# Optimization experiments

Hardware: AMD Instinct MI355X
Metric: run time of the kernel (lower is better)

Reference implementation:

```python
import jax, jax.numpy as jnp
import numpy as np

N = 1_000_000      # level-0 points
M = 50_000         # level-1 superpoints
G = 16             # graphs in batch (norm_index groups)
DIMS = (32, 128, 64)
EPS = 1e-5
NEG_SLOPE = 0.01   # torch nn.LeakyReLU default


def graph_norm(x, idx, gamma, beta, num_graphs):
    """Per-graph batch norm ('graph' mode): normalize each feature channel
    using mean/var computed over the nodes of each graph (segment)."""
    cnt = jax.ops.segment_sum(jnp.ones((x.shape[0],), x.dtype), idx, num_segments=num_graphs)
    cnt = jnp.maximum(cnt, 1.0)[:, None]                       # [G,1]
    mean = jax.ops.segment_sum(x, idx, num_segments=num_graphs) / cnt      # [G,D]
    ex2 = jax.ops.segment_sum(x * x, idx, num_segments=num_graphs) / cnt   # [G,D]
    var = jnp.maximum(ex2 - mean * mean, 0.0)
    xn = (x - mean[idx]) * jax.lax.rsqrt(var[idx] + EPS)       # gather stats back to nodes
    return xn * gamma + beta


def setup_inputs() -> dict:
    key = jax.random.key(0)
    ks = jax.random.split(key, 8)
    d0, d1, d2 = DIMS
    x = jax.random.normal(ks[0], (N, d0), dtype=jnp.float32)
    W1 = jax.random.normal(ks[1], (d1, d0), dtype=jnp.float32) * (1.0 / np.sqrt(d0))
    b1 = jnp.zeros((d1,), jnp.float32)
    g1 = jnp.ones((d1,), jnp.float32)
    beta1 = jnp.zeros((d1,), jnp.float32)
    W2 = jax.random.normal(ks[2], (d2, d1), dtype=jnp.float32) * (1.0 / np.sqrt(d1))
    b2 = jnp.zeros((d2,), jnp.float32)
    g2 = jnp.ones((d2,), jnp.float32)
    beta2 = jnp.zeros((d2,), jnp.float32)
    norm_index = jnp.sort(jax.random.randint(ks[3], (N,), 0, G)).astype(jnp.int64)
    super_index = jax.random.randint(ks[4], (N,), 0, M).astype(jnp.int64)
    return {"x": x, "W1": W1, "b1": b1, "g1": g1, "beta1": beta1,
            "W2": W2, "b2": b2, "g2": g2, "beta2": beta2,
            "norm_index": norm_index, "super_index": super_index}


def reference(x, W1, b1, g1, beta1, W2, b2, g2, beta2, norm_index, super_index):
    # MLP layer 1: Linear -> graph BatchNorm -> LeakyReLU
    h = jnp.dot(x, W1.T) + b1                                  # [N,128]
    h = jax.nn.leaky_relu(graph_norm(h, norm_index, g1, beta1, G), NEG_SLOPE)
    # MLP layer 2
    h = jnp.dot(h, W2.T) + b2                                  # [N,64]
    h = jax.nn.leaky_relu(graph_norm(h, norm_index, g2, beta2, G), NEG_SLOPE)
    # level == 0: scatter-max pooling into level-1 superpoints
    out = jax.ops.segment_max(h, super_index, num_segments=M)  # [M,64]
    # torch_scatter leaves empty segments at 0; segment_max gives -inf
    out = jnp.where(jnp.isneginf(out), 0.0, out)
    return out
```

## Files before the change

kernel.cpp:

```cpp
#include <hip/hip_runtime.h>
#include <hip/hip_bf16.h>
#include <stdint.h>

#define NGRAPH 16
#define EPSV 1e-5f
#define SLOPE 0.01f

#define OFF_S1   0
#define OFF_CNT  512
#define OFF_SUM2 528
#define OFF_SQ2  1552
#define ZERO_SMALL 2576
#define OFF_A1   2576
#define OFF_C1   4624
#define OFF_A2   6672
#define OFF_C2   7696
#define OFF_M    16384
#define M_FLOATS 16384
#define H2_BYTE_OFF 65536

typedef __attribute__((ext_vector_type(4))) float f32x4;
typedef __attribute__((ext_vector_type(8))) short short8v;

__device__ __forceinline__ unsigned int enc_f32(float f) {
  unsigned int b = __float_as_uint(f);
  return (b & 0x80000000u) ? ~b : (b | 0x80000000u);
}
__device__ __forceinline__ unsigned int f2bf_bits(float f) {
  unsigned int u = __float_as_uint(f);
  unsigned int r = u + 0x7FFFu + ((u >> 16) & 1u);
  return r >> 16;
}
__device__ __forceinline__ float bfround(float f) {
  unsigned int u = __float_as_uint(f);
  unsigned int r = (u + 0x7FFFu + ((u >> 16) & 1u)) & 0xFFFF0000u;
  return __uint_as_float(r);
}

__global__ void k_zero_all(float* __restrict__ ws, int* __restrict__ hist, int M) {
  int i = blockIdx.x * 256 + threadIdx.x;
  if (i < ZERO_SMALL) ws[i] = 0.0f;
  if (i < M_FLOATS) ws[OFF_M + i] = 0.0f;
  if (i < M) hist[i] = 0;
}

__global__ void k_init_out(unsigned int* __restrict__ out, int n) {
  int i = blockIdx.x * 256 + threadIdx.x;
  if (i < n) out[i] = 0u;
}

__global__ __launch_bounds__(256) void k1_mom(
    const float* __restrict__ x, const int* __restrict__ gidx,
    float* __restrict__ ws, int N) {
  const int tid = threadIdx.x;
  const int gw = blockIdx.x * 4 + (tid >> 6);
  const int l = tid & 63;
  const int bi = l >> 3, bj = l & 7;
  const bool diag = (bi == bj);
  const bool isL0 = (l == 0);
  const int nwaves = gridDim.x * 4;
  const int npw = (N + nwaves - 1) / nwaves;
  const int n0 = gw * npw;
  const int n1 = min(n0 + npw, N);

  float m00,m01,m02,m03,m10,m11,m12,m13,m20,m21,m22,m23,m30,m31,m32,m33;
  m00=m01=m02=m03=m10=m11=m12=m13=m20=m21=m22=m23=m30=m31=m32=m33=0.f;
  float sv0=0.f, sv1=0.f, sv2=0.f, sv3=0.f, cnt=0.f;
  int curg = -1;

  if (n0 < n1) {
    const int nlast = n1 - 1;
    int g = gidx[n0];
    float4 pi = *(const float4*)(x + (size_t)n0 * 32 + bi * 4);
    float4 pj = *(const float4*)(x + (size_t)n0 * 32 + bj * 4);
    #pragma unroll 1
    for (int n = n0; n < n1; ++n) {
      const int nn = min(n + 1, nlast);
      const int g2 = gidx[nn];
      float4 pi2 = *(const float4*)(x + (size_t)nn * 32 + bi * 4);
      float4 pj2 = *(const float4*)(x + (size_t)nn * 32 + bj * 4);
      if (g != curg) {
        if (curg >= 0) {
          float* Mg = ws + OFF_M + curg * 1024 + bi * 4 * 32 + bj * 4;
          atomicAdd(Mg + 0*32 + 0, m00); atomicAdd(Mg + 0*32 + 1, m01);
          atomicAdd(Mg + 0*32 + 2, m02); atomicAdd(Mg + 0*32 + 3, m03);
          atomicAdd(Mg + 1*32 + 0, m10); atomicAdd(Mg + 1*32 + 1, m11);
          atomicAdd(Mg + 1*32 + 2, m12); atomicAdd(Mg + 1*32 + 3, m13);
          atomicAdd(Mg + 2*32 + 0, m20); atomicAdd(Mg + 2*32 + 1, m21);
          atomicAdd(Mg + 2*32 + 2, m22); atomicAdd(Mg + 2*32 + 3, m23);
          atomicAdd(Mg + 3*32 + 0, m30); atomicAdd(Mg + 3*32 + 1, m31);
          atomicAdd(Mg + 3*32 + 2, m32); atomicAdd(Mg + 3*32 + 3, m33);
          if (diag) {
            float* Sg = ws + OFF_S1 + curg * 32 + bi * 4;
            atomicAdd(Sg + 0, sv0); atomicAdd(Sg + 1, sv1);
            atomicAdd(Sg + 2, sv2); atomicAdd(Sg + 3, sv3);
          }
          if (isL0) atomicAdd(ws + OFF_CNT + curg, cnt);
        }
        curg = g;
        m00=m01=m02=m03=m10=m11=m12=m13=m20=m21=m22=m23=m30=m31=m32=m33=0.f;
        sv0=sv1=sv2=sv3=0.f; cnt=0.f;
      }
      float xi0 = bfround(pi.x), xi1 = bfround(pi.y), xi2 = bfround(pi.z), xi3 = bfround(pi.w);
      float xj0 = bfround(pj.x), xj1 = bfround(pj.y), xj2 = bfround(pj.z), xj3 = bfround(pj.w);
      m00 = fmaf(xi0,xj0,m00); m01 = fmaf(xi0,xj1,m01); m02 = fmaf(xi0,xj2,m02); m03 = fmaf(xi0,xj3,m03);
      m10 = fmaf(xi1,xj0,m10); m11 = fmaf(xi1,xj1,m11); m12 = fmaf(xi1,xj2,m12); m13 = fmaf(xi1,xj3,m13);
      m20 = fmaf(xi2,xj0,m20); m21 = fmaf(xi2,xj1,m21); m22 = fmaf(xi2,xj2,m22); m23 = fmaf(xi2,xj3,m23);
      m30 = fmaf(xi3,xj0,m30); m31 = fmaf(xi3,xj1,m31); m32 = fmaf(xi3,xj2,m32); m33 = fmaf(xi3,xj3,m33);
      if (diag) { sv0 += xi0; sv1 += xi1; sv2 += xi2; sv3 += xi3; }
      cnt += 1.f;
      pi = pi2; pj = pj2; g = g2;
    }
  }
  if (curg >= 0) {
    float* Mg = ws + OFF_M + curg * 1024 + bi * 4 * 32 + bj * 4;
    atomicAdd(Mg + 0*32 + 0, m00); atomicAdd(Mg + 0*32 + 1, m01);
    atomicAdd(Mg + 0*32 + 2, m02); atomicAdd(Mg + 0*32 + 3, m03);
    atomicAdd(Mg + 1*32 + 0, m10); atomicAdd(Mg + 1*32 + 1, m11);
    atomicAdd(Mg + 1*32 + 2, m12); atomicAdd(Mg + 1*32 + 3, m13);
    atomicAdd(Mg + 2*32 + 0, m20); atomicAdd(Mg + 2*32 + 1, m21);
    atomicAdd(Mg + 2*32 + 2, m22); atomicAdd(Mg + 2*32 + 3, m23);
    atomicAdd(Mg + 3*32 + 0, m30); atomicAdd(Mg + 3*32 + 1, m31);
    atomicAdd(Mg + 3*32 + 2, m32); atomicAdd(Mg + 3*32 + 3, m33);
    if (diag) {
      float* Sg = ws + OFF_S1 + curg * 32 + bi * 4;
      atomicAdd(Sg + 0, sv0); atomicAdd(Sg + 1, sv1);
      atomicAdd(Sg + 2, sv2); atomicAdd(Sg + 3, sv3);
    }
    if (isL0) atomicAdd(ws + OFF_CNT + curg, cnt);
  }
}

__global__ __launch_bounds__(128) void k2a_fin1(
    const float* __restrict__ W1, const float* __restrict__ b1,
    const float* __restrict__ g1, const float* __restrict__ be1,
    float* __restrict__ ws) {
  __shared__ float Ms[1024];
  __shared__ float ss[32];
  __shared__ float cs;
  const int g = blockIdx.x, c = threadIdx.x;
  for (int i = c; i < 1024; i += 128) Ms[i] = ws[OFF_M + g * 1024 + i];
  if (c < 32) ss[c] = ws[OFF_S1 + g * 32 + c];
  if (c == 0) cs = fmaxf(ws[OFF_CNT + g], 1.0f);
  __syncthreads();
  float w[32];
  #pragma unroll
  for (int k = 0; k < 32; ++k) w[k] = bfround(W1[c * 32 + k]);
  float dot = 0.f;
  #pragma unroll
  for (int k = 0; k < 32; ++k) dot = fmaf(w[k], ss[k], dot);
  float quad = 0.f;
  #pragma unroll 1
  for (int i = 0; i < 32; ++i) {
    const float* Mr = Ms + i * 32;
    float acc = 0.f;
    #pragma unroll
    for (int j = 0; j < 32; ++j) acc = fmaf(Mr[j], w[j], acc);
    quad = fmaf(w[i], acc, quad);
  }
  const float cnt = cs;
  const float bc = b1[c];
  const float mean = dot / cnt + bc;
  const float e2 = (quad + 2.f * bc * dot) / cnt + bc * bc;
  const float var = fmaxf(e2 - mean * mean, 0.0f);
  const float a = rsqrtf(var + EPSV) * g1[c];
  ws[OFF_A1 + g * 128 + c] = a;
  ws[OFF_C1 + g * 128 + c] = fmaf(a, bc - mean, be1[c]);
}

__global__ void k2_fin(float* __restrict__ ws, const float* __restrict__ gamma,
                       const float* __restrict__ beta, int D, int off_sum,
                       int off_sq, int off_a, int off_c) {
  int i = blockIdx.x * 256 + threadIdx.x;
  if (i >= NGRAPH * D) return;
  int g = i / D, c = i % D;
  float cnt  = fmaxf(ws[OFF_CNT + g], 1.0f);
  float mean = ws[off_sum + i] / cnt;
  float ex2  = ws[off_sq + i] / cnt;
  float var  = fmaxf(ex2 - mean * mean, 0.0f);
  float a = rsqrtf(var + EPSV) * gamma[c];
  ws[off_a + i] = a;
  ws[off_c + i] = fmaf(-mean, a, beta[c]);
}

__global__ __launch_bounds__(256) void k3_mfma(
    const float* __restrict__ x, const float* __restrict__ W1,
    const float* __restrict__ W2, const float* __restrict__ b2,
    const int* __restrict__ gidx, float* __restrict__ ws,
    unsigned short* __restrict__ h2out, int N, int ntiles, int tpw) {
  __shared__ float a1s[2048];
  __shared__ float c1s[2048];
  __shared__ __align__(16) unsigned short h1t[4][2048];
  const int tid = threadIdx.x;
  const int wv = tid >> 6;
  const int l = tid & 63;
  const int ln = l & 15;
  const int kq = l >> 4;

  for (int i = tid; i < 2048; i += 256) { a1s[i] = ws[OFF_A1 + i]; c1s[i] = ws[OFF_C1 + i]; }

  short8v w1f[8];
  #pragma unroll
  for (int t = 0; t < 8; ++t) {
    const float* wr = W1 + (size_t)(t * 16 + ln) * 32 + kq * 8;
    float4 p = *(const float4*)wr, q = *(const float4*)(wr + 4);
    short8v f;
    f[0] = (short)f2bf_bits(p.x); f[1] = (short)f2bf_bits(p.y);
    f[2] = (short)f2bf_bits(p.z); f[3] = (short)f2bf_bits(p.w);
    f[4] = (short)f2bf_bits(q.x); f[5] = (short)f2bf_bits(q.y);
    f[6] = (short)f2bf_bits(q.z); f[7] = (short)f2bf_bits(q.w);
    w1f[t] = f;
  }
  short8v w2f[4][4];
  #pragma unroll
  for (int ct = 0; ct < 4; ++ct)
    #pragma unroll
    for (int kt = 0; kt < 4; ++kt) {
      const float* wr = W2 + (size_t)(ct * 16 + ln) * 128 + kt * 32 + kq * 8;
      float4 p = *(const float4*)wr, q = *(const float4*)(wr + 4);
      short8v f;
      f[0] = (short)f2bf_bits(p.x); f[1] = (short)f2bf_bits(p.y);
      f[2] = (short)f2bf_bits(p.z); f[3] = (short)f2bf_bits(p.w);
      f[4] = (short)f2bf_bits(q.x); f[5] = (short)f2bf_bits(q.y);
      f[6] = (short)f2bf_bits(q.z); f[7] = (short)f2bf_bits(q.w);
      w2f[ct][kt] = f;
    }
  float b2v[4];
  #pragma unroll
  for (int ct = 0; ct < 4; ++ct) b2v[ct] = b2[ct * 16 + ln];
  __syncthreads();

  const int gw = blockIdx.x * 4 + wv;
  const int t0 = gw * tpw;
  const int t1 = min(t0 + tpw, ntiles);
  if (t0 >= t1) return;

  unsigned short* myt = &h1t[wv][0];
  const f32x4 zero4 = {0.f, 0.f, 0.f, 0.f};
  float s2[4] = {0.f, 0.f, 0.f, 0.f}, q2a[4] = {0.f, 0.f, 0.f, 0.f};
  int curg2 = -1;

  float4 p, q;
  int gg[4];
  {
    const int base = t0 * 16;
    const float* xr = x + (size_t)min(base + ln, N - 1) * 32 + kq * 8;
    p = *(const float4*)xr; q = *(const float4*)(xr + 4);
    #pragma unroll
    for (int i = 0; i < 4; ++i) gg[i] = gidx[min(base + kq * 4 + i, N - 1)];
  }

  #pragma unroll 1
  for (int t = t0; t < t1; ++t) {
    const int base = t * 16;
    float4 p2, q2;
    int gg2[4];
    {
      const int nb = min(t + 1, t1 - 1) * 16;
      const float* xr = x + (size_t)min(nb + ln, N - 1) * 32 + kq * 8;
      p2 = *(const float4*)xr; q2 = *(const float4*)(xr + 4);
      #pragma unroll
      for (int i = 0; i < 4; ++i) gg2[i] = gidx[min(nb + kq * 4 + i, N - 1)];
    }
    short8v af;
    af[0] = (short)f2bf_bits(p.x); af[1] = (short)f2bf_bits(p.y);
    af[2] = (short)f2bf_bits(p.z); af[3] = (short)f2bf_bits(p.w);
    af[4] = (short)f2bf_bits(q.x); af[5] = (short)f2bf_bits(q.y);
    af[6] = (short)f2bf_bits(q.z); af[7] = (short)f2bf_bits(q.w);
    f32x4 acc1[8];
    #pragma unroll
    for (int tt = 0; tt < 8; ++tt)
      acc1[tt] = __builtin_amdgcn_mfma_f32_16x16x32_bf16(af, w1f[tt], zero4, 0, 0, 0);
    #pragma unroll
    for (int tt = 0; tt < 8; ++tt) {
      const int ct_ = tt * 16 + ln;
      #pragma unroll
      for (int i = 0; i < 4; ++i) {
        const float a = a1s[gg[i] * 128 + ct_];
        const float cc = c1s[gg[i] * 128 + ct_];
        float v = fmaf(acc1[tt][i], a, cc);
        v = v >= 0.f ? v : v * SLOPE;
        const int row = kq * 4 + i;
        const int byte = (row * 256 + ct_ * 2) ^ ((row & 7) << 4);
        *(unsigned short*)((char*)myt + byte) = (unsigned short)f2bf_bits(v);
      }
    }
    asm volatile("s_waitcnt lgkmcnt(0)" ::: "memory");
    __builtin_amdgcn_sched_barrier(0);
    short8v a2f[4];
    #pragma unroll
    for (int kt = 0; kt < 4; ++kt) {
      const int byte = (ln * 256 + kt * 64 + kq * 16) ^ ((ln & 7) << 4);
      a2f[kt] = *(const short8v*)((const char*)myt + byte);
    }
    f32x4 acc2[4];
    #pragma unroll
    for (int ct = 0; ct < 4; ++ct) {
      f32x4 a = zero4;
      #pragma unroll
      for (int kt = 0; kt < 4; ++kt)
        a = __builtin_amdgcn_mfma_f32_16x16x32_bf16(a2f[kt], w2f[ct][kt], a, 0, 0, 0);
      acc2[ct] = a;
    }
    #pragma unroll
    for (int i = 0; i < 4; ++i) {
      const int node = base + kq * 4 + i;
      if (node >= N) break;
      const int g = gg[i];
      if (g != curg2) {
        if (curg2 >= 0) {
          #pragma unroll
          for (int ct = 0; ct < 4; ++ct) {
            atomicAdd(ws + OFF_SUM2 + curg2 * 64 + ct * 16 + ln, s2[ct]);
            atomicAdd(ws + OFF_SQ2  + curg2 * 64 + ct * 16 + ln, q2a[ct]);
          }
        }
        curg2 = g;
        #pragma unroll
        for (int ct = 0; ct < 4; ++ct) { s2[ct] = 0.f; q2a[ct] = 0.f; }
      }
      #pragma unroll
      for (int ct = 0; ct < 4; ++ct) {
        const float v2 = acc2[ct][i] + b2v[ct];
        s2[ct] += v2; q2a[ct] = fmaf(v2, v2, q2a[ct]);
        h2out[(size_t)node * 64 + ct * 16 + ln] = (unsigned short)f2bf_bits(v2);
      }
    }
    p = p2; q = q2;
    #pragma unroll
    for (int i = 0; i < 4; ++i) gg[i] = gg2[i];
  }
  if (curg2 >= 0) {
    #pragma unroll
    for (int ct = 0; ct < 4; ++ct) {
      atomicAdd(ws + OFF_SUM2 + curg2 * 64 + ct * 16 + ln, s2[ct]);
      atomicAdd(ws + OFF_SQ2  + curg2 * 64 + ct * 16 + ln, q2a[ct]);
    }
  }
}

__global__ void k5a_hist(const int* __restrict__ sidx, int* __restrict__ hist, int N) {
  int n = blockIdx.x * 256 + threadIdx.x;
  if (n < N) atomicAdd(&hist[sidx[n]], 1);
}

__global__ __launch_bounds__(256) void k5b_scan(
    const int* __restrict__ hist, int* __restrict__ offsets,
    int* __restrict__ cursor, int M, int N) {
  __shared__ int part[256];
  const int tid = threadIdx.x;
  const int chunk = (M + 255) / 256;
  const int lo = min(tid * chunk, M), hi = min(lo + chunk, M);
  int s = 0;
  for (int i = lo; i < hi; ++i) s += hist[i];
  part[tid] = s;
  __syncthreads();
  if (tid == 0) {
    int run = 0;
    for (int i = 0; i < 256; ++i) { int v = part[i]; part[i] = run; run += v; }
  }
  __syncthreads();
  int run = part[tid];
  for (int i = lo; i < hi; ++i) {
    int v = hist[i];
    offsets[i] = run; cursor[i] = run; run += v;
  }
  if (tid == 255) offsets[M] = N;
}

__global__ void k5c_perm(const int* __restrict__ sidx, const int* __restrict__ gidx,
                         int* __restrict__ cursor, int* __restrict__ perm, int N) {
  int n = blockIdx.x * 256 + threadIdx.x;
  if (n >= N) return;
  int sp = sidx[n];
  int pos = atomicAdd(&cursor[sp], 1);
  perm[pos] = (n << 4) | (gidx[n] & 15);
}

__global__ __launch_bounds__(256) void k5d_gather(
    const unsigned short* __restrict__ h2, const int* __restrict__ perm,
    const int* __restrict__ offsets, const float* __restrict__ ws,
    float* __restrict__ out, int M) {
  __shared__ float a2s[1024], c2s[1024];
  const int tid = threadIdx.x;
  for (int i = tid; i < 1024; i += 256) { a2s[i] = ws[OFF_A2 + i]; c2s[i] = ws[OFF_C2 + i]; }
  __syncthreads();
  const int seg = blockIdx.x * 4 + (tid >> 6);
  if (seg >= M) return;
  const int lane = tid & 63;
  const int lo = offsets[seg], hi = offsets[seg + 1];
  float acc = -3.402823466e38f;
  if (hi > lo) {
    const int last = hi - 1;
    int pc = perm[lo];
    unsigned short hc = h2[(size_t)(pc >> 4) * 64 + lane];
    int pn = perm[min(lo + 1, last)];
    #pragma unroll 1
    for (int i = lo; i < hi; ++i) {
      const unsigned short hn = h2[(size_t)(pn >> 4) * 64 + lane];
      const int pn2 = perm[min(i + 2, last)];
      const int g = pc & 15;
      const float v = __uint_as_float((unsigned int)hc << 16);
      float y = fmaf(v, a2s[g * 64 + lane], c2s[g * 64 + lane]);
      y = y >= 0.f ? y : y * SLOPE;
      acc = fmaxf(acc, y);
      pc = pn; hc = hn; pn = pn2;
    }
  }
  out[(size_t)seg * 64 + lane] = (hi > lo) ? acc : 0.0f;
}

__global__ __launch_bounds__(256) void k5_scatter(
    const unsigned int* __restrict__ h2, const int* __restrict__ gidx,
    const int* __restrict__ sidx, const float* __restrict__ ws,
    unsigned int* __restrict__ out, int N) {
  int t = blockIdx.x * 256 + threadIdx.x;
  int node = t >> 4;
  if (node >= N) return;
  int jq = t & 15, j = jq * 4;
  int g = gidx[node];
  int sp = sidx[node];
  float4 av = *(const float4*)(ws + OFF_A2 + g * 64 + j);
  float4 cv = *(const float4*)(ws + OFF_C2 + g * 64 + j);
  uint2 hv = *(const uint2*)(h2 + (size_t)node * 32 + jq * 2);
  float v0 = __uint_as_float(hv.x << 16);
  float v1 = __uint_as_float(hv.x & 0xFFFF0000u);
  float v2 = __uint_as_float(hv.y << 16);
  float v3 = __uint_as_float(hv.y & 0xFFFF0000u);
  v0 = fmaf(v0, av.x, cv.x); v0 = v0 >= 0.f ? v0 : v0 * SLOPE;
  v1 = fmaf(v1, av.y, cv.y); v1 = v1 >= 0.f ? v1 : v1 * SLOPE;
  v2 = fmaf(v2, av.z, cv.z); v2 = v2 >= 0.f ? v2 : v2 * SLOPE;
  v3 = fmaf(v3, av.w, cv.w); v3 = v3 >= 0.f ? v3 : v3 * SLOPE;
  unsigned int* o = out + (size_t)sp * 64 + j;
  atomicMax(o + 0, enc_f32(v0));
  atomicMax(o + 1, enc_f32(v1));
  atomicMax(o + 2, enc_f32(v2));
  atomicMax(o + 3, enc_f32(v3));
}

__global__ void k6_decode(unsigned int* __restrict__ o, int n) {
  int i = blockIdx.x * 256 + threadIdx.x;
  if (i >= n) return;
  unsigned int e = o[i];
  float f;
  if (e == 0u) f = 0.0f;
  else if (e & 0x80000000u) f = __uint_as_float(e ^ 0x80000000u);
  else f = __uint_as_float(~e);
  ((float*)o)[i] = f;
}

extern "C" void kernel_launch(void* const* d_in, const int* in_sizes, int n_in,
                              void* d_out, int out_size, void* d_ws, size_t ws_size,
                              hipStream_t stream) {
  const float* x   = (const float*)d_in[0];
  const float* W1  = (const float*)d_in[1];
  const float* b1  = (const float*)d_in[2];
  const float* g1  = (const float*)d_in[3];
  const float* be1 = (const float*)d_in[4];
  const float* W2  = (const float*)d_in[5];
  const float* b2  = (const float*)d_in[6];
  const float* g2  = (const float*)d_in[7];
  const float* be2 = (const float*)d_in[8];
  const int* gidx  = (const int*)d_in[9];
  const int* sidx  = (const int*)d_in[10];
  const int N = in_sizes[9];
  const int M = out_size / 64;
  float* ws = (float*)d_ws;
  unsigned short* h2 = (unsigned short*)((char*)d_ws + H2_BYTE_OFF);
  unsigned int* out_u = (unsigned int*)d_out;

  const size_t idx_off = (size_t)H2_BYTE_OFF + (size_t)N * 128;
  int* hist    = (int*)((char*)d_ws + idx_off);
  int* cursor  = hist + M;
  int* offsets = cursor + M;
  int* perm    = offsets + M + 1;
  const size_t needed_fast = idx_off + (size_t)(3 * M + 1 + N) * 4;
  const bool fast = (ws_size >= needed_fast);

  const int zmax = (M_FLOATS > M ? M_FLOATS : M);
  hipLaunchKernelGGL(k_zero_all, dim3((zmax + 255) / 256), dim3(256), 0, stream,
                     ws, hist, fast ? M : 0);
  hipLaunchKernelGGL(k1_mom, dim3(1024), dim3(256), 0, stream, x, gidx, ws, N);
  hipLaunchKernelGGL(k2a_fin1, dim3(NGRAPH), dim3(128), 0, stream, W1, b1, g1, be1, ws);
  if (fast) {
    hipLaunchKernelGGL(k5a_hist, dim3((N + 255) / 256), dim3(256), 0, stream, sidx, hist, N);
    hipLaunchKernelGGL(k5b_scan, dim3(1), dim3(256), 0, stream, hist, offsets, cursor, M, N);
    hipLaunchKernelGGL(k5c_perm, dim3((N + 255) / 256), dim3(256), 0, stream,
                       sidx, gidx, cursor, perm, N);
  }
  const int ntiles = (N + 15) / 16;
  const int NW = 4096;
  const int tpw = (ntiles + NW - 1) / NW;
  const int k3blocks = (ntiles + 4 * tpw - 1) / (4 * tpw);
  hipLaunchKernelGGL(k3_mfma, dim3(k3blocks), dim3(256), 0, stream,
                     x, W1, W2, b2, gidx, ws, h2, N, ntiles, tpw);
  hipLaunchKernelGGL(k2_fin, dim3((NGRAPH * 64 + 255) / 256), dim3(256), 0, stream,
                     ws, g2, be2, 64, OFF_SUM2, OFF_SQ2, OFF_A2, OFF_C2);
  if (fast) {
    hipLaunchKernelGGL(k5d_gather, dim3((M + 3) / 4), dim3(256), 0, stream,
                       h2, perm, offsets, ws, (float*)d_out, M);
  } else {
    hipLaunchKernelGGL(k_init_out, dim3((out_size + 255) / 256), dim3(256), 0, stream,
                       out_u, out_size);
    hipLaunchKernelGGL(k5_scatter, dim3((N * 16 + 255) / 256), dim3(256), 0, stream,
                       (const unsigned int*)h2, gidx, sidx, ws, out_u, N);
    hipLaunchKernelGGL(k6_decode, dim3((out_size + 255) / 256), dim3(256), 0, stream,
                       out_u, out_size);
  }
}
```

Before: 1.031 ms.

## Use MFMA for moment accumulation, double-buffer k3 LDS, split layer-2 stats kernel

The first-layer second-moment matrix (x^T x per graph) is now accumulated with 32x32x16 bf16 MFMA over 16-node chunks instead of scalar FMAs, with a masked two-pass path for chunks that span graph boundaries. The fused MLP kernel is restructured into a produce/consume software pipeline with double-buffered LDS, transposed MFMA operands, packed bf16 conversion and vectorized stores. Its per-node group-stat atomics are moved into a new k4_stats2 kernel that re-reads h2. Grid sizes change as well. This trades an extra pass over h2 for a leaner main kernel.

```diff
diff --git a/kernel.cpp b/kernel.cpp
--- a/kernel.cpp
+++ b/kernel.cpp
@@ -20,8 +20,16 @@
 #define H2_BYTE_OFF 65536
 
 typedef __attribute__((ext_vector_type(4))) float f32x4;
+typedef __attribute__((ext_vector_type(16))) float f32x16;
 typedef __attribute__((ext_vector_type(8))) short short8v;
 
+union pk4 { unsigned int u[4]; short8v v; };
+
+__device__ __forceinline__ unsigned int cvtpk(float lo, float hi) {
+  unsigned int r;
+  asm("v_cvt_pk_bf16_f32 %0, %1, %2" : "=v"(r) : "v"(lo), "v"(hi));
+  return r;
+}
 __device__ __forceinline__ unsigned int enc_f32(float f) {
   unsigned int b = __float_as_uint(f);
   return (b & 0x80000000u) ? ~b : (b | 0x80000000u);
@@ -35,6 +43,9 @@
   unsigned int u = __float_as_uint(f);
   unsigned int r = (u + 0x7FFFu + ((u >> 16) & 1u)) & 0xFFFF0000u;
   return __uint_as_float(r);
+}
+__device__ __forceinline__ float leaky(float v) {
+  return fmaxf(v, 0.f) + SLOPE * fminf(v, 0.f);
 }
 
 __global__ void k_zero_all(float* __restrict__ ws, int* __restrict__ hist, int M) {
@@ -55,80 +66,102 @@
   const int tid = threadIdx.x;
   const int gw = blockIdx.x * 4 + (tid >> 6);
   const int l = tid & 63;
-  const int bi = l >> 3, bj = l & 7;
-  const bool diag = (bi == bj);
-  const bool isL0 = (l == 0);
+  const int ch = l & 31;
+  const int half = l >> 5;
+  const int nchunks = (N + 15) / 16;
   const int nwaves = gridDim.x * 4;
-  const int npw = (N + nwaves - 1) / nwaves;
-  const int n0 = gw * npw;
-  const int n1 = min(n0 + npw, N);
-
-  float m00,m01,m02,m03,m10,m11,m12,m13,m20,m21,m22,m23,m30,m31,m32,m33;
-  m00=m01=m02=m03=m10=m11=m12=m13=m20=m21=m22=m23=m30=m31=m32=m33=0.f;
-  float sv0=0.f, sv1=0.f, sv2=0.f, sv3=0.f, cnt=0.f;
+  const int cpw = (nchunks + nwaves - 1) / nwaves;
+  const int c0 = gw * cpw;
+  const int c1 = min(c0 + cpw, nchunks);
+  if (c0 >= c1) return;
+
+  f32x16 acc;
+  #pragma unroll
+  for (int r = 0; r < 16; ++r) acc[r] = 0.f;
+  float sv = 0.f, cnt = 0.f;
   int curg = -1;
 
-  if (n0 < n1) {
-    const int nlast = n1 - 1;
-    int g = gidx[n0];
-    float4 pi = *(const float4*)(x + (size_t)n0 * 32 + bi * 4);
-    float4 pj = *(const float4*)(x + (size_t)n0 * 32 + bj * 4);
-    #pragma unroll 1
-    for (int n = n0; n < n1; ++n) {
-      const int nn = min(n + 1, nlast);
-      const int g2 = gidx[nn];
-      float4 pi2 = *(const float4*)(x + (size_t)nn * 32 + bi * 4);
-      float4 pj2 = *(const float4*)(x + (size_t)nn * 32 + bj * 4);
-      if (g != curg) {
-        if (curg >= 0) {
-          float* Mg = ws + OFF_M + curg * 1024 + bi * 4 * 32 + bj * 4;
-          atomicAdd(Mg + 0*32 + 0, m00); atomicAdd(Mg + 0*32 + 1, m01);
-          atomicAdd(Mg + 0*32 + 2, m02); atomicAdd(Mg + 0*32 + 3, m03);
-          atomicAdd(Mg + 1*32 + 0, m10); atomicAdd(Mg + 1*32 + 1, m11);
-          atomicAdd(Mg + 1*32 + 2, m12); atomicAdd(Mg + 1*32 + 3, m13);
-          atomicAdd(Mg + 2*32 + 0, m20); atomicAdd(Mg + 2*32 + 1, m21);
-          atomicAdd(Mg + 2*32 + 2, m22); atomicAdd(Mg + 2*32 + 3, m23);
-          atomicAdd(Mg + 3*32 + 0, m30); atomicAdd(Mg + 3*32 + 1, m31);
-          atomicAdd(Mg + 3*32 + 2, m32); atomicAdd(Mg + 3*32 + 3, m33);
-          if (diag) {
-            float* Sg = ws + OFF_S1 + curg * 32 + bi * 4;
-            atomicAdd(Sg + 0, sv0); atomicAdd(Sg + 1, sv1);
-            atomicAdd(Sg + 2, sv2); atomicAdd(Sg + 3, sv3);
+  auto loadc = [&](int c, float* v, int& g0, int& gl) {
+    const int nb = c * 16;
+    #pragma unroll
+    for (int e = 0; e < 8; ++e) {
+      const int node = nb + half * 8 + e;
+      v[e] = (node < N) ? x[(size_t)node * 32 + ch] : 0.f;
+    }
+    g0 = gidx[nb];
+    gl = gidx[min(nb + 15, N - 1)];
+  };
+  auto flush = [&](int g) {
+    float* Mg = ws + OFF_M + g * 1024;
+    #pragma unroll
+    for (int r = 0; r < 16; ++r) {
+      const int row = (r & 3) + 8 * (r >> 2) + 4 * half;
+      atomicAdd(Mg + row * 32 + ch, acc[r]);
+      acc[r] = 0.f;
+    }
+    atomicAdd(ws + OFF_S1 + g * 32 + ch, sv);
+    if (l == 0) atomicAdd(ws + OFF_CNT + g, cnt);
+    sv = 0.f; cnt = 0.f;
+  };
+
+  float v[8]; int g0, gl;
+  loadc(c0, v, g0, gl);
+  #pragma unroll 1
+  for (int c = c0; c < c1; ++c) {
+    float v2[8]; int g02, gl2;
+    loadc(min(c + 1, c1 - 1), v2, g02, gl2);
+    if (g0 != curg) { if (curg >= 0) flush(curg); curg = g0; }
+    const int nb = c * 16;
+    if (g0 == gl && nb + 16 <= N) {
+      pk4 P;
+      P.u[0] = cvtpk(v[0], v[1]); P.u[1] = cvtpk(v[2], v[3]);
+      P.u[2] = cvtpk(v[4], v[5]); P.u[3] = cvtpk(v[6], v[7]);
+      acc = __builtin_amdgcn_mfma_f32_32x32x16_bf16(P.v, P.v, acc, 0, 0, 0);
+      #pragma unroll
+      for (int e = 0; e < 4; ++e) {
+        sv += __uint_as_float(P.u[e] << 16);
+        sv += __uint_as_float(P.u[e] & 0xFFFF0000u);
+      }
+      if (l == 0) cnt += 16.f;
+    } else {
+      int ge[8];
+      #pragma unroll
+      for (int e = 0; e < 8; ++e)
+        ge[e] = gidx[min(nb + half * 8 + e, N - 1)];
+      #pragma unroll 1
+      for (int pass = 0; pass < 2; ++pass) {
+        if (pass == 1) { if (gl == g0) break; flush(g0); curg = gl; }
+        const int tg = (pass == 0) ? g0 : gl;
+        float mv[8];
+        #pragma unroll
+        for (int e = 0; e < 8; ++e) {
+          const int node = nb + half * 8 + e;
+          mv[e] = (node < N && ge[e] == tg) ? v[e] : 0.f;
+        }
+        pk4 P;
+        P.u[0] = cvtpk(mv[0], mv[1]); P.u[1] = cvtpk(mv[2], mv[3]);
+        P.u[2] = cvtpk(mv[4], mv[5]); P.u[3] = cvtpk(mv[6], mv[7]);
+        acc = __builtin_amdgcn_mfma_f32_32x32x16_bf16(P.v, P.v, acc, 0, 0, 0);
+        #pragma unroll
+        for (int e = 0; e < 4; ++e) {
+          sv += __uint_as_float(P.u[e] << 16);
+          sv += __uint_as_float(P.u[e] & 0xFFFF0000u);
+        }
+        if (l == 0) {
+          float cc = 0.f;
+          for (int i2 = 0; i2 < 16; ++i2) {
+            const int node = nb + i2;
+            if (node < N && gidx[node] == tg) cc += 1.f;
           }
-          if (isL0) atomicAdd(ws + OFF_CNT + curg, cnt);
+          cnt += cc;
         }
-        curg = g;
-        m00=m01=m02=m03=m10=m11=m12=m13=m20=m21=m22=m23=m30=m31=m32=m33=0.f;
-        sv0=sv1=sv2=sv3=0.f; cnt=0.f;
       }
-      float xi0 = bfround(pi.x), xi1 = bfround(pi.y), xi2 = bfround(pi.z), xi3 = bfround(pi.w);
-      float xj0 = bfround(pj.x), xj1 = bfround(pj.y), xj2 = bfround(pj.z), xj3 = bfround(pj.w);
-      m00 = fmaf(xi0,xj0,m00); m01 = fmaf(xi0,xj1,m01); m02 = fmaf(xi0,xj2,m02); m03 = fmaf(xi0,xj3,m03);
-      m10 = fmaf(xi1,xj0,m10); m11 = fmaf(xi1,xj1,m11); m12 = fmaf(xi1,xj2,m12); m13 = fmaf(xi1,xj3,m13);
-      m20 = fmaf(xi2,xj0,m20); m21 = fmaf(xi2,xj1,m21); m22 = fmaf(xi2,xj2,m22); m23 = fmaf(xi2,xj3,m23);
-      m30 = fmaf(xi3,xj0,m30); m31 = fmaf(xi3,xj1,m31); m32 = fmaf(xi3,xj2,m32); m33 = fmaf(xi3,xj3,m33);
-      if (diag) { sv0 += xi0; sv1 += xi1; sv2 += xi2; sv3 += xi3; }
-      cnt += 1.f;
-      pi = pi2; pj = pj2; g = g2;
-    }
-  }
-  if (curg >= 0) {
-    float* Mg = ws + OFF_M + curg * 1024 + bi * 4 * 32 + bj * 4;
-    atomicAdd(Mg + 0*32 + 0, m00); atomicAdd(Mg + 0*32 + 1, m01);
-    atomicAdd(Mg + 0*32 + 2, m02); atomicAdd(Mg + 0*32 + 3, m03);
-    atomicAdd(Mg + 1*32 + 0, m10); atomicAdd(Mg + 1*32 + 1, m11);
-    atomicAdd(Mg + 1*32 + 2, m12); atomicAdd(Mg + 1*32 + 3, m13);
-    atomicAdd(Mg + 2*32 + 0, m20); atomicAdd(Mg + 2*32 + 1, m21);
-    atomicAdd(Mg + 2*32 + 2, m22); atomicAdd(Mg + 2*32 + 3, m23);
-    atomicAdd(Mg + 3*32 + 0, m30); atomicAdd(Mg + 3*32 + 1, m31);
-    atomicAdd(Mg + 3*32 + 2, m32); atomicAdd(Mg + 3*32 + 3, m33);
-    if (diag) {
-      float* Sg = ws + OFF_S1 + curg * 32 + bi * 4;
-      atomicAdd(Sg + 0, sv0); atomicAdd(Sg + 1, sv1);
-      atomicAdd(Sg + 2, sv2); atomicAdd(Sg + 3, sv3);
-    }
-    if (isL0) atomicAdd(ws + OFF_CNT + curg, cnt);
-  }
+    }
+    #pragma unroll
+    for (int e = 0; e < 8; ++e) v[e] = v2[e];
+    g0 = g02; gl = gl2;
+  }
+  if (curg >= 0) flush(curg);
 }
 
 __global__ __launch_bounds__(128) void k2a_fin1(
@@ -186,16 +219,14 @@
 __global__ __launch_bounds__(256) void k3_mfma(
     const float* __restrict__ x, const float* __restrict__ W1,
     const float* __restrict__ W2, const float* __restrict__ b2,
-    const int* __restrict__ gidx, float* __restrict__ ws,
+    const int* __restrict__ gidx, const float* __restrict__ ws,
     unsigned short* __restrict__ h2out, int N, int ntiles, int tpw) {
   __shared__ float a1s[2048];
   __shared__ float c1s[2048];
-  __shared__ __align__(16) unsigned short h1t[4][2048];
-  const int tid = threadIdx.x;
-  const int wv = tid >> 6;
-  const int l = tid & 63;
-  const int ln = l & 15;
-  const int kq = l >> 4;
+  __shared__ __align__(16) unsigned short h1d[4][2][2048];
+  const int tid = threadIdx.x, wv = tid >> 6, l = tid & 63;
+  const int ln = l & 15, kq = l >> 4;
+  const int swz = (ln & 7) << 4;
 
   for (int i = tid; i < 2048; i += 256) { a1s[i] = ws[OFF_A1 + i]; c1s[i] = ws[OFF_C1 + i]; }
 
@@ -225,9 +256,12 @@
       f[6] = (short)f2bf_bits(q.z); f[7] = (short)f2bf_bits(q.w);
       w2f[ct][kt] = f;
     }
-  float b2v[4];
+  float b2v[16];
   #pragma unroll
-  for (int ct = 0; ct < 4; ++ct) b2v[ct] = b2[ct * 16 + ln];
+  for (int ct = 0; ct < 4; ++ct)
+    #pragma unroll
+    for (int i = 0; i < 4; ++i)
+      b2v[ct * 4 + i] = b2[ct * 16 + kq * 4 + i];
   __syncthreads();
 
   const int gw = blockIdx.x * 4 + wv;
@@ -235,63 +269,46 @@
   const int t1 = min(t0 + tpw, ntiles);
   if (t0 >= t1) return;
 
-  unsigned short* myt = &h1t[wv][0];
+  unsigned short* br = &h1d[wv][0][0];
+  unsigned short* bw = &h1d[wv][1][0];
   const f32x4 zero4 = {0.f, 0.f, 0.f, 0.f};
-  float s2[4] = {0.f, 0.f, 0.f, 0.f}, q2a[4] = {0.f, 0.f, 0.f, 0.f};
-  int curg2 = -1;
-
-  float4 p, q;
-  int gg[4];
-  {
-    const int base = t0 * 16;
-    const float* xr = x + (size_t)min(base + ln, N - 1) * 32 + kq * 8;
-    p = *(const float4*)xr; q = *(const float4*)(xr + 4);
-    #pragma unroll
-    for (int i = 0; i < 4; ++i) gg[i] = gidx[min(base + kq * 4 + i, N - 1)];
-  }
-
-  #pragma unroll 1
-  for (int t = t0; t < t1; ++t) {
-    const int base = t * 16;
-    float4 p2, q2;
-    int gg2[4];
-    {
-      const int nb = min(t + 1, t1 - 1) * 16;
-      const float* xr = x + (size_t)min(nb + ln, N - 1) * 32 + kq * 8;
-      p2 = *(const float4*)xr; q2 = *(const float4*)(xr + 4);
-      #pragma unroll
-      for (int i = 0; i < 4; ++i) gg2[i] = gidx[min(nb + kq * 4 + i, N - 1)];
-    }
-    short8v af;
-    af[0] = (short)f2bf_bits(p.x); af[1] = (short)f2bf_bits(p.y);
-    af[2] = (short)f2bf_bits(p.z); af[3] = (short)f2bf_bits(p.w);
-    af[4] = (short)f2bf_bits(q.x); af[5] = (short)f2bf_bits(q.y);
-    af[6] = (short)f2bf_bits(q.z); af[7] = (short)f2bf_bits(q.w);
+
+  auto loadT = [&](int t, float4& P, float4& Q, int& G) {
+    const int node = min(t * 16 + ln, N - 1);
+    const float* xr = x + (size_t)node * 32 + kq * 8;
+    P = *(const float4*)xr; Q = *(const float4*)(xr + 4);
+    G = gidx[node];
+  };
+  auto produce = [&](float4 P, float4 Q, int G, unsigned short* dst) {
+    pk4 A;
+    A.u[0] = cvtpk(P.x, P.y); A.u[1] = cvtpk(P.z, P.w);
+    A.u[2] = cvtpk(Q.x, Q.y); A.u[3] = cvtpk(Q.z, Q.w);
     f32x4 acc1[8];
     #pragma unroll
     for (int tt = 0; tt < 8; ++tt)
-      acc1[tt] = __builtin_amdgcn_mfma_f32_16x16x32_bf16(af, w1f[tt], zero4, 0, 0, 0);
+      acc1[tt] = __builtin_amdgcn_mfma_f32_16x16x32_bf16(w1f[tt], A.v, zero4, 0, 0, 0);
+    const float* ap = a1s + G * 128;
+    const float* cp = c1s + G * 128;
     #pragma unroll
     for (int tt = 0; tt < 8; ++tt) {
-      const int ct_ = tt * 16 + ln;
-      #pragma unroll
-      for (int i = 0; i < 4; ++i) {
-        const float a = a1s[gg[i] * 128 + ct_];
-        const float cc = c1s[gg[i] * 128 + ct_];
-        float v = fmaf(acc1[tt][i], a, cc);
-        v = v >= 0.f ? v : v * SLOPE;
-        const int row = kq * 4 + i;
-        const int byte = (row * 256 + ct_ * 2) ^ ((row & 7) << 4);
-        *(unsigned short*)((char*)myt + byte) = (unsigned short)f2bf_bits(v);
-      }
-    }
-    asm volatile("s_waitcnt lgkmcnt(0)" ::: "memory");
-    __builtin_amdgcn_sched_barrier(0);
+      const int ch0 = tt * 16 + kq * 4;
+      f32x4 av = *(const f32x4*)(ap + ch0);
+      f32x4 cv = *(const f32x4*)(cp + ch0);
+      float v0 = leaky(fmaf(acc1[tt][0], av[0], cv[0]));
+      float v1 = leaky(fmaf(acc1[tt][1], av[1], cv[1]));
+      float v2 = leaky(fmaf(acc1[tt][2], av[2], cv[2]));
+      float v3 = leaky(fmaf(acc1[tt][3], av[3], cv[3]));
+      uint2 w; w.x = cvtpk(v0, v1); w.y = cvtpk(v2, v3);
+      const int off = (ln * 256 + ch0 * 2) ^ swz;
+      *(uint2*)&dst[off >> 1] = w;
+    }
+  };
+  auto consume = [&](int t, const unsigned short* src) {
     short8v a2f[4];
     #pragma unroll
     for (int kt = 0; kt < 4; ++kt) {
-      const int byte = (ln * 256 + kt * 64 + kq * 16) ^ ((ln & 7) << 4);
-      a2f[kt] = *(const short8v*)((const char*)myt + byte);
+      const int off = (ln * 256 + kt * 64 + kq * 16) ^ swz;
+      a2f[kt] = *(const short8v*)&src[off >> 1];
     }
     f32x4 acc2[4];
     #pragma unroll
@@ -299,43 +316,78 @@
       f32x4 a = zero4;
       #pragma unroll
       for (int kt = 0; kt < 4; ++kt)
-        a = __builtin_amdgcn_mfma_f32_16x16x32_bf16(a2f[kt], w2f[ct][kt], a, 0, 0, 0);
+        a = __builtin_amdgcn_mfma_f32_16x16x32_bf16(w2f[ct][kt], a2f[kt], a, 0, 0, 0);
       acc2[ct] = a;
     }
-    #pragma unroll
-    for (int i = 0; i < 4; ++i) {
-      const int node = base + kq * 4 + i;
-      if (node >= N) break;
-      const int g = gg[i];
-      if (g != curg2) {
-        if (curg2 >= 0) {
-          #pragma unroll
-          for (int ct = 0; ct < 4; ++ct) {
-            atomicAdd(ws + OFF_SUM2 + curg2 * 64 + ct * 16 + ln, s2[ct]);
-            atomicAdd(ws + OFF_SQ2  + curg2 * 64 + ct * 16 + ln, q2a[ct]);
-          }
-        }
-        curg2 = g;
-        #pragma unroll
-        for (int ct = 0; ct < 4; ++ct) { s2[ct] = 0.f; q2a[ct] = 0.f; }
-      }
+    const int node = t * 16 + ln;
+    if (node < N) {
+      unsigned short* orow = h2out + (size_t)node * 64;
       #pragma unroll
       for (int ct = 0; ct < 4; ++ct) {
-        const float v2 = acc2[ct][i] + b2v[ct];
-        s2[ct] += v2; q2a[ct] = fmaf(v2, v2, q2a[ct]);
-        h2out[(size_t)node * 64 + ct * 16 + ln] = (unsigned short)f2bf_bits(v2);
+        float u0 = acc2[ct][0] + b2v[ct * 4 + 0];
+        float u1 = acc2[ct][1] + b2v[ct * 4 + 1];
+        float u2 = acc2[ct][2] + b2v[ct * 4 + 2];
+        float u3 = acc2[ct][3] + b2v[ct * 4 + 3];
+        uint2 w; w.x = cvtpk(u0, u1); w.y = cvtpk(u2, u3);
+        *(uint2*)&orow[ct * 16 + kq * 4] = w;
       }
     }
-    p = p2; q = q2;
-    #pragma unroll
-    for (int i = 0; i < 4; ++i) gg[i] = gg2[i];
-  }
-  if (curg2 >= 0) {
-    #pragma unroll
-    for (int ct = 0; ct < 4; ++ct) {
-      atomicAdd(ws + OFF_SUM2 + curg2 * 64 + ct * 16 + ln, s2[ct]);
-      atomicAdd(ws + OFF_SQ2  + curg2 * 64 + ct * 16 + ln, q2a[ct]);
-    }
+  };
+
+  float4 p, q; int gv;
+  loadT(t0, p, q, gv);
+  float4 p2, q2; int gv2;
+  loadT(min(t0 + 1, t1 - 1), p2, q2, gv2);
+  produce(p, q, gv, br);
+  #pragma unroll 1
+  for (int t = t0; t < t1; ++t) {
+    if (t + 1 < t1) {
+      float4 p3, q3; int gv3;
+      loadT(min(t + 2, t1 - 1), p3, q3, gv3);
+      produce(p2, q2, gv2, bw);
+      p2 = p3; q2 = q3; gv2 = gv3;
+    }
+    consume(t, br);
+    unsigned short* tmp = br; br = bw; bw = tmp;
+  }
+}
+
+__global__ __launch_bounds__(256) void k4_stats2(
+    const unsigned short* __restrict__ h2, const int* __restrict__ gidx,
+    float* __restrict__ ws, int N) {
+  const int tid = threadIdx.x;
+  const int gw = blockIdx.x * 4 + (tid >> 6);
+  const int lane = tid & 63;
+  const int nwaves = gridDim.x * 4;
+  const int npw = (N + nwaves - 1) / nwaves;
+  const int n0 = gw * npw;
+  const int n1 = min(n0 + npw, N);
+  float s = 0.f, qq = 0.f;
+  int curg = -1;
+  if (n0 < n1) {
+    const int nlast = n1 - 1;
+    int g = gidx[n0];
+    unsigned short hv = h2[(size_t)n0 * 64 + lane];
+    #pragma unroll 1
+    for (int n = n0; n < n1; ++n) {
+      const int nn = min(n + 1, nlast);
+      const int g2 = gidx[nn];
+      const unsigned short hv2 = h2[(size_t)nn * 64 + lane];
+      if (g != curg) {
+        if (curg >= 0) {
+          atomicAdd(ws + OFF_SUM2 + curg * 64 + lane, s);
+          atomicAdd(ws + OFF_SQ2  + curg * 64 + lane, qq);
+        }
+        curg = g; s = 0.f; qq = 0.f;
+      }
+      const float v = __uint_as_float((unsigned int)hv << 16);
+      s += v; qq = fmaf(v, v, qq);
+      g = g2; hv = hv2;
+    }
+  }
+  if (curg >= 0) {
+    atomicAdd(ws + OFF_SUM2 + curg * 64 + lane, s);
+    atomicAdd(ws + OFF_SQ2  + curg * 64 + lane, qq);
   }
 }
 
@@ -480,7 +532,7 @@
   const int zmax = (M_FLOATS > M ? M_FLOATS : M);
   hipLaunchKernelGGL(k_zero_all, dim3((zmax + 255) / 256), dim3(256), 0, stream,
                      ws, hist, fast ? M : 0);
-  hipLaunchKernelGGL(k1_mom, dim3(1024), dim3(256), 0, stream, x, gidx, ws, N);
+  hipLaunchKernelGGL(k1_mom, dim3(256), dim3(256), 0, stream, x, gidx, ws, N);
   hipLaunchKernelGGL(k2a_fin1, dim3(NGRAPH), dim3(128), 0, stream, W1, b1, g1, be1, ws);
   if (fast) {
     hipLaunchKernelGGL(k5a_hist, dim3((N + 255) / 256), dim3(256), 0, stream, sidx, hist, N);
@@ -489,11 +541,12 @@
                        sidx, gidx, cursor, perm, N);
   }
   const int ntiles = (N + 15) / 16;
-  const int NW = 4096;
-  const int tpw = (ntiles + NW - 1) / NW;
+  const int NW3 = 3072;
+  const int tpw = (ntiles + NW3 - 1) / NW3;
   const int k3blocks = (ntiles + 4 * tpw - 1) / (4 * tpw);
   hipLaunchKernelGGL(k3_mfma, dim3(k3blocks), dim3(256), 0, stream,
                      x, W1, W2, b2, gidx, ws, h2, N, ntiles, tpw);
+  hipLaunchKernelGGL(k4_stats2, dim3(512), dim3(256), 0, stream, h2, gidx, ws, N);
   hipLaunchKernelGGL(k2_fin, dim3((NGRAPH * 64 + 255) / 256), dim3(256), 0, stream,
                      ws, g2, be2, 64, OFF_SUM2, OFF_SQ2, OFF_A2, OFF_C2);
   if (fast) {
```

Measured after the change: 910.5 us. 11.7% less time.
